# Performance work log

Measured on AMD Instinct MI355X. Metric: run time of the kernel, lower is better.

## Reference

```python
import jax, jax.numpy as jnp
import numpy as np

N_NODES = 50000
HEADS = 4
CH = 128
NEG_SLOPE = 0.2


def _gatv2_layer(x, src, dst, Wl, Wr, att, bias):
    # x: [N, Fin]; src/dst: [E'] (self-loops already appended)
    N = x.shape[0]
    xl = (x @ Wl).reshape(N, HEADS, CH)   # source-side transform
    xr = (x @ Wr).reshape(N, HEADS, CH)   # target-side transform
    e = jax.nn.leaky_relu(xl[src] + xr[dst], NEG_SLOPE)   # [E', H, C]
    logits = jnp.einsum('ehc,hc->eh', e, att)             # [E', H]
    # segment softmax over incoming edges of each destination node
    m = jax.ops.segment_max(logits, dst, num_segments=N)
    m = jnp.where(jnp.isfinite(m), m, 0.0)
    p = jnp.exp(logits - m[dst])
    denom = jax.ops.segment_sum(p, dst, num_segments=N)
    alpha = p / denom[dst]                                # [E', H]
    out = jax.ops.segment_sum(alpha[:, :, None] * xl[src], dst, num_segments=N)
    return out.reshape(N, HEADS * CH) + bias


def setup_inputs() -> dict:
    key = jax.random.key(0)
    ks = jax.random.split(key, 12)
    E = 400000
    x = jax.random.normal(ks[0], (N_NODES, 55), dtype=jnp.float32)
    edge_index = jax.random.randint(ks[1], (2, E), 0, N_NODES, dtype=jnp.int64)
    s = 0.1
    d1, d2 = 55, HEADS * CH
    return {
        'x': x,
        'edge_index': edge_index,
        'W1l': jax.random.normal(ks[2], (d1, d2), dtype=jnp.float32) * s,
        'W1r': jax.random.normal(ks[3], (d1, d2), dtype=jnp.float32) * s,
        'att1': jax.random.normal(ks[4], (HEADS, CH), dtype=jnp.float32) * s,
        'b1': jnp.zeros((d2,), dtype=jnp.float32),
        'W2l': jax.random.normal(ks[5], (d2, d2), dtype=jnp.float32) * s,
        'W2r': jax.random.normal(ks[6], (d2, d2), dtype=jnp.float32) * s,
        'att2': jax.random.normal(ks[7], (HEADS, CH), dtype=jnp.float32) * s,
        'b2': jnp.zeros((d2,), dtype=jnp.float32),
        'Wc': jax.random.normal(ks[8], (d2, 49), dtype=jnp.float32) * s,
        'bc': jnp.zeros((49,), dtype=jnp.float32),
    }


def reference(x, edge_index, W1l, W1r, att1, b1, W2l, W2r, att2, b2, Wc, bc):
    # add self loops once (PyG GATv2Conv default add_self_loops=True)
    loops = jnp.arange(N_NODES, dtype=edge_index.dtype)
    src = jnp.concatenate([edge_index[0], loops])
    dst = jnp.concatenate([edge_index[1], loops])
    h = _gatv2_layer(x, src, dst, W1l, W1r, att1, b1)
    h = jax.nn.elu(h)  # dropout is identity in eval mode
    h = _gatv2_layer(h, src, dst, W2l, W2r, att2, b2)
    h = jax.nn.elu(h)
    # forward applies conv2 a second time (conv3 unused in source)
    h = _gatv2_layer(h, src, dst, W2l, W2r, att2, b2)
    h = jax.nn.elu(h)
    return h @ Wc + bc
```

## Files before the change

### kernel.cpp

```cpp
#include <hip/hip_runtime.h>
#include <hip/hip_bf16.h>

constexpr int NN   = 50000;
constexpr int EE   = 400000;
constexpr int EP   = 450000;
constexpr int D    = 512;
constexpr int D2   = 1024;
constexpr int F0   = 55;
constexpr int F0P  = 64;
constexpr int OUTC = 49;

typedef __hip_bfloat16 bf16;

using frag_ab  = __attribute__((ext_vector_type(8))) short;
using frag_cd4 = __attribute__((ext_vector_type(4))) float;

__device__ inline void stf(float* p, float v) { *p = v; }
__device__ inline void stf(bf16* p, float v)  { *p = __float2bfloat16(v); }

__device__ inline void unpack8(uint4 u, float* f) {
    unsigned w[4] = {u.x, u.y, u.z, u.w};
    #pragma unroll
    for (int j = 0; j < 4; ++j) {
        __hip_bfloat162 h = *(__hip_bfloat162*)&w[j];
        float2 t = __bfloat1622float2(h);
        f[2 * j] = t.x; f[2 * j + 1] = t.y;
    }
}

template <typename TC, int NS>
__global__ __launch_bounds__(512, 4) void gemm_dp(
    const bf16* __restrict__ A,
    const bf16* __restrict__ Bt,
    TC* __restrict__ C,
    const float* __restrict__ bias,
    int M, int Ncs)
{
    constexpr int K  = NS * 32;
    constexpr int BM = 256, BN = 128, BK = 32;
    __shared__ __align__(16) bf16 As[3][BM * BK];
    __shared__ __align__(16) bf16 Bs[3][BN * BK];

    int bx = blockIdx.x, by = blockIdx.y;
    if (gridDim.x == 8) {
        int bid = by * 8 + bx;
        bx = (bid >> 3) & 7;
        by = (bid & 7) + ((bid >> 6) << 3);
    }
    if (by * BM >= M) return;

    const int tid = threadIdx.x;
    const int w   = tid >> 6;
    const int l   = tid & 63;
    const int rowBase = by * BM;
    const int colBase = bx * BN;

    const bf16* gA[2];
    #pragma unroll
    for (int j = 0; j < 2; ++j) {
        int f = j * 512 + tid;
        int row = f >> 2, c = (f & 3) ^ ((row >> 1) & 3);
        int ar = rowBase + row; if (ar >= M) ar = M - 1;
        gA[j] = A + (size_t)ar * K + c * 8;
    }
    const bf16* gB;
    {
        int f = tid;
        int row = f >> 2, c = (f & 3) ^ ((row >> 1) & 3);
        gB = Bt + (size_t)(colBase + row) * K + c * 8;
    }

    const int l15 = l & 15, l4 = l >> 4;
    const int wm = (w >> 1) * 64;
    const int wn = (w & 1) * 64;
    int aoff[4], boff[4];
    #pragma unroll
    for (int i = 0; i < 4; ++i) {
        int ra = wm + i * 16 + l15;
        int rb = wn + i * 16 + l15;
        aoff[i] = ra * BK + ((l4 ^ ((ra >> 1) & 3)) * 8);
        boff[i] = rb * BK + ((l4 ^ ((rb >> 1) & 3)) * 8);
    }

    frag_cd4 acc[4][4] = {};

    auto stage = [&](int s) {
        int slot = s % 3;
        __builtin_amdgcn_global_load_lds(
            (const __attribute__((address_space(1))) void*)(gA[0] + s * BK),
            (__attribute__((address_space(3))) void*)(&As[slot][(w * 64) * 8]),
            16, 0, 0);
        __builtin_amdgcn_global_load_lds(
            (const __attribute__((address_space(1))) void*)(gA[1] + s * BK),
            (__attribute__((address_space(3))) void*)(&As[slot][(512 + w * 64) * 8]),
            16, 0, 0);
        __builtin_amdgcn_global_load_lds(
            (const __attribute__((address_space(1))) void*)(gB + s * BK),
            (__attribute__((address_space(3))) void*)(&Bs[slot][(w * 64) * 8]),
            16, 0, 0);
    };

    stage(0);
    if (NS > 1) stage(1);

    #pragma unroll
    for (int s = 0; s < NS; ++s) {
        if (s + 1 < NS) asm volatile("s_waitcnt vmcnt(3)" ::: "memory");
        else            asm volatile("s_waitcnt vmcnt(0)" ::: "memory");
        __builtin_amdgcn_s_barrier();
        asm volatile("" ::: "memory");

        if (s + 2 < NS) stage(s + 2);

        const bf16* Ab = As[s % 3];
        const bf16* Bb = Bs[s % 3];
        frag_ab a[4], b[4];
        #pragma unroll
        for (int i = 0; i < 4; ++i) a[i] = *(const frag_ab*)&Ab[aoff[i]];
        #pragma unroll
        for (int n = 0; n < 4; ++n) b[n] = *(const frag_ab*)&Bb[boff[n]];

        __builtin_amdgcn_s_setprio(1);
        #pragma unroll
        for (int i = 0; i < 4; ++i)
            #pragma unroll
            for (int n = 0; n < 4; ++n)
                acc[i][n] = __builtin_amdgcn_mfma_f32_16x16x32_bf16(
                    a[i], b[n], acc[i][n], 0, 0, 0);
        __builtin_amdgcn_s_setprio(0);
    }

    #pragma unroll
    for (int mi = 0; mi < 4; ++mi) {
        #pragma unroll
        for (int r = 0; r < 4; ++r) {
            int row = rowBase + wm + mi * 16 + l4 * 4 + r;
            if (row >= M) continue;
            #pragma unroll
            for (int ni = 0; ni < 4; ++ni) {
                int col = colBase + wn + ni * 16 + l15;
                if (col >= Ncs) continue;
                float v = acc[mi][ni][r];
                if (bias) v += bias[col];
                stf(&C[(size_t)row * Ncs + col], v);
            }
        }
    }
}

__global__ void convert_transpose2(const float* __restrict__ W0,
                                   const float* __restrict__ W1,
                                   bf16* __restrict__ Wt) {
    __shared__ float tile[32][33];
    const float* W = blockIdx.z ? W1 : W0;
    bf16* dst = Wt + (size_t)blockIdx.z * D * D;
    int bn = blockIdx.x * 32, bk = blockIdx.y * 32;
    int tx = threadIdx.x & 31, ty = threadIdx.x >> 5;
    #pragma unroll
    for (int i = 0; i < 32; i += 8)
        tile[ty + i][tx] = W[(size_t)(bk + ty + i) * D + bn + tx];
    __syncthreads();
    #pragma unroll
    for (int i = 0; i < 32; i += 8)
        dst[(size_t)(bn + ty + i) * D + bk + tx] = __float2bfloat16(tile[tx][ty + i]);
}

__global__ void pad_convert_x(const float* __restrict__ x, bf16* __restrict__ Xp) {
    int idx = blockIdx.x * blockDim.x + threadIdx.x;
    if (idx >= NN * F0P) return;
    int n = idx >> 6, t = idx & 63;
    float v = (t < F0) ? x[n * F0 + t] : 0.f;
    Xp[idx] = __float2bfloat16(v);
}

__global__ void conv_transpose_w1(const float* __restrict__ Wl,
                                  const float* __restrict__ Wr,
                                  bf16* __restrict__ Wt) {
    const float* W = blockIdx.y ? Wr : Wl;
    bf16* dst = Wt + (size_t)blockIdx.y * D * F0P;
    int n = blockIdx.x;
    int k = threadIdx.x;
    float v = (k < F0) ? W[(size_t)k * D + n] : 0.f;
    dst[n * F0P + k] = __float2bfloat16(v);
}

__global__ void conv_transpose_wc(const float* __restrict__ W, bf16* __restrict__ Wt) {
    int n = blockIdx.x;
    for (int k = threadIdx.x; k < D; k += blockDim.x) {
        float v = (n < OUTC) ? W[(size_t)k * OUTC + n] : 0.f;
        Wt[(size_t)n * D + k] = __float2bfloat16(v);
    }
}

__global__ void zero_ints(int* __restrict__ p, int n) {
    int i = blockIdx.x * blockDim.x + threadIdx.x;
    if (i < n) p[i] = 0;
}

__global__ void count_dst(const int* __restrict__ dstIdx, int* __restrict__ cnt) {
    int e = blockIdx.x * blockDim.x + threadIdx.x;
    if (e >= EP) return;
    int dst = (e < EE) ? dstIdx[e] : (e - EE);
    atomicAdd(&cnt[dst], 1);
}

__global__ void scan_blocks(const int* __restrict__ cnt, int* __restrict__ off,
                            int* __restrict__ bsum) {
    __shared__ int sh[1024];
    int i = blockIdx.x * 1024 + threadIdx.x;
    int v = (i < NN) ? cnt[i] : 0;
    sh[threadIdx.x] = v;
    __syncthreads();
    #pragma unroll
    for (int d = 1; d < 1024; d <<= 1) {
        int t = (threadIdx.x >= d) ? sh[threadIdx.x - d] : 0;
        __syncthreads();
        sh[threadIdx.x] += t;
        __syncthreads();
    }
    if (i < NN) off[i] = sh[threadIdx.x] - v;
    if (threadIdx.x == 1023) bsum[blockIdx.x] = sh[1023];
}

__global__ void scan_bsums(int* __restrict__ bsum, int* __restrict__ bbase,
                           int* __restrict__ off, int nb) {
    int lane = threadIdx.x;
    int orig = (lane < nb) ? bsum[lane] : 0;
    int v = orig;
    #pragma unroll
    for (int d = 1; d < 64; d <<= 1) {
        int t = __shfl_up(v, d);
        if (lane >= d) v += t;
    }
    if (lane < nb) bbase[lane] = v - orig;
    if (lane == 63) off[NN] = v;
}

__global__ void add_base(int* __restrict__ off, const int* __restrict__ bbase) {
    int i = blockIdx.x * 1024 + threadIdx.x;
    if (blockIdx.x == 0 || i >= NN) return;
    off[i] += bbase[blockIdx.x];
}

__global__ void fill_srcpos(const int* __restrict__ srcIdx, const int* __restrict__ dstIdx,
                            const int* __restrict__ off, int* __restrict__ cnt,
                            int* __restrict__ srcPos) {
    int e = blockIdx.x * blockDim.x + threadIdx.x;
    if (e >= EP) return;
    int dst = (e < EE) ? dstIdx[e] : (e - EE);
    int src = (e < EE) ? srcIdx[e] : (e - EE);
    int pos = off[dst] + atomicAdd(&cnt[dst], 1);
    srcPos[pos] = src;
}

__global__ __launch_bounds__(256) void gat_edge_fused(
    const bf16* __restrict__ XLR, const float* __restrict__ att,
    const int* __restrict__ off, const int* __restrict__ srcPos,
    const float* __restrict__ bias, bf16* __restrict__ Hout)
{
    int v = blockIdx.x * 4 + (threadIdx.x >> 6);
    if (v >= NN) return;
    int lane = threadIdx.x & 63;

    uint4 ru = *(const uint4*)(XLR + (size_t)v * D2 + D + lane * 8);
    float xr[8]; unpack8(ru, xr);
    const float4* a4 = (const float4*)(att + lane * 8);
    float4 aa = a4[0], ab = a4[1];
    float at[8] = {aa.x, aa.y, aa.z, aa.w, ab.x, ab.y, ab.z, ab.w};

    int s0 = off[v], s1 = off[v + 1];
    float den = 0.f;
    float acc[8] = {};

    uint4 lb0 = {0, 0, 0, 0}, lb1 = {0, 0, 0, 0};
    if (s0 < s1)     lb0 = *(const uint4*)(XLR + (size_t)srcPos[s0] * D2 + lane * 8);
    if (s0 + 1 < s1) lb1 = *(const uint4*)(XLR + (size_t)srcPos[s0 + 1] * D2 + lane * 8);

    for (int i = s0; i < s1; ++i) {
        uint4 cur = lb0;
        lb0 = lb1;
        if (i + 2 < s1)
            lb1 = *(const uint4*)(XLR + (size_t)srcPos[i + 2] * D2 + lane * 8);

        float xl[8]; unpack8(cur, xl);
        float sa = 0.f, sb = 0.f;
        #pragma unroll
        for (int j = 0; j < 4; ++j) {
            float t = xl[j] + xr[j];
            t = fmaxf(t, 0.2f * t);
            sa = fmaf(t, at[j], sa);
        }
        #pragma unroll
        for (int j = 4; j < 8; ++j) {
            float t = xl[j] + xr[j];
            t = fmaxf(t, 0.2f * t);
            sb = fmaf(t, at[j], sb);
        }
        float s = sa + sb;
        s += __shfl_xor(s, 1);
        s += __shfl_xor(s, 2);
        s += __shfl_xor(s, 4);
        s += __shfl_xor(s, 8);
        s = fminf(fmaxf(s, -60.f), 60.f);
        float p = __expf(s);
        den += p;
        #pragma unroll
        for (int j = 0; j < 8; ++j) acc[j] = fmaf(p, xl[j], acc[j]);
    }
    float r = 1.f / den;

    const float4* b4 = (const float4*)(bias + lane * 8);
    float4 ba = b4[0], bb = b4[1];
    float bi[8] = {ba.x, ba.y, ba.z, ba.w, bb.x, bb.y, bb.z, bb.w};
    uint4 ou;
    unsigned* ow = (unsigned*)&ou;
    #pragma unroll
    for (int j = 0; j < 4; ++j) {
        float o0 = acc[2 * j] * r + bi[2 * j];
        float o1 = acc[2 * j + 1] * r + bi[2 * j + 1];
        o0 = o0 > 0.f ? o0 : (__expf(o0) - 1.f);
        o1 = o1 > 0.f ? o1 : (__expf(o1) - 1.f);
        __hip_bfloat162 h{__float2bfloat16(o0), __float2bfloat16(o1)};
        ow[j] = *(unsigned*)&h;
    }
    *(uint4*)(Hout + (size_t)v * D + lane * 8) = ou;
}

extern "C" void kernel_launch(void* const* d_in, const int* in_sizes, int n_in,
                              void* d_out, int out_size, void* d_ws, size_t ws_size,
                              hipStream_t stream) {
    const float* x    = (const float*)d_in[0];
    const int*   ei   = (const int*)d_in[1];
    const float* W1l  = (const float*)d_in[2];
    const float* W1r  = (const float*)d_in[3];
    const float* att1 = (const float*)d_in[4];
    const float* b1   = (const float*)d_in[5];
    const float* W2l  = (const float*)d_in[6];
    const float* W2r  = (const float*)d_in[7];
    const float* att2 = (const float*)d_in[8];
    const float* b2   = (const float*)d_in[9];
    const float* Wc   = (const float*)d_in[10];
    const float* bc   = (const float*)d_in[11];
    float* out = (float*)d_out;

    const int* srcIdx = ei;
    const int* dstIdx = ei + EE;

    constexpr int NB = (NN + 1023) / 1024;

    bf16* XLR  = (bf16*)d_ws;
    bf16* Hb   = XLR + (size_t)NN * D2;
    bf16* Xpad = Hb + (size_t)NN * D;
    bf16* W2T  = Xpad + (size_t)NN * F0P;
    bf16* W1T  = W2T + (size_t)D2 * D;
    bf16* WcT  = W1T + (size_t)D2 * F0P;
    int* cnt   = (int*)(WcT + (size_t)128 * D);
    int* cnt2  = cnt + NN;
    int* off   = cnt2 + NN;
    int* srcPos= off + (NN + 1);
    int* bsum  = srcPos + EP;
    int* bbase = bsum + NB;

    zero_ints<<<(2 * NN + 255) / 256, 256, 0, stream>>>(cnt, 2 * NN);
    count_dst<<<(EP + 255) / 256, 256, 0, stream>>>(dstIdx, cnt);
    scan_blocks<<<NB, 1024, 0, stream>>>(cnt, off, bsum);
    scan_bsums<<<1, 64, 0, stream>>>(bsum, bbase, off, NB);
    add_base<<<NB, 1024, 0, stream>>>(off, bbase);
    fill_srcpos<<<(EP + 255) / 256, 256, 0, stream>>>(srcIdx, dstIdx, off, cnt2, srcPos);

    dim3 ctGrid(D / 32, D / 32, 2);
    convert_transpose2<<<ctGrid, 256, 0, stream>>>(W2l, W2r, W2T);
    dim3 w1Grid(D, 2);
    conv_transpose_w1<<<w1Grid, F0P, 0, stream>>>(W1l, W1r, W1T);
    conv_transpose_wc<<<128, 256, 0, stream>>>(Wc, WcT);
    pad_convert_x<<<(NN * F0P + 255) / 256, 256, 0, stream>>>(x, Xpad);

    int panels = (NN + 255) / 256;
    int gy = (panels + 7) / 8 * 8;
    dim3 gemmGrid(D2 / 128, gy);
    int nodeBlocks = (NN + 3) / 4;

    gemm_dp<bf16, 2><<<gemmGrid, 512, 0, stream>>>(Xpad, W1T, XLR, nullptr, NN, D2);
    gat_edge_fused<<<nodeBlocks, 256, 0, stream>>>(XLR, att1, off, srcPos, b1, Hb);

    for (int rep = 0; rep < 2; ++rep) {
        gemm_dp<bf16, 16><<<gemmGrid, 512, 0, stream>>>(Hb, W2T, XLR, nullptr, NN, D2);
        gat_edge_fused<<<nodeBlocks, 256, 0, stream>>>(XLR, att2, off, srcPos, b2, Hb);
    }

    dim3 gridc(1, panels);
    gemm_dp<float, 16><<<gridc, 512, 0, stream>>>(Hb, WcT, out, bc, NN, OUTC);
}
```

Before: 565.9 us.

## Split GAT edge kernel per head, four nodes per wavefront

The edge aggregation kernel now gives each 16-lane group one attention head of one node, so each wavefront covers four nodes on the same head. Block IDs are swizzled so that paired blocks handle different heads of the same node range, which aims to cut per-wave serialization on high-degree nodes and improve L2 locality for gathered source rows. The trade-off is narrower gathers (256 bytes per row per group instead of 1 KB), more divergence from unequal degrees within a wave, and a hard-coded grid size.

```diff
diff --git a/kernel.cpp b/kernel.cpp
--- a/kernel.cpp
+++ b/kernel.cpp
@@ -253,18 +253,24 @@
     srcPos[pos] = src;
 }
 
-__global__ __launch_bounds__(256) void gat_edge_fused(
+__global__ __launch_bounds__(256) void gat_edge_head(
     const bf16* __restrict__ XLR, const float* __restrict__ att,
     const int* __restrict__ off, const int* __restrict__ srcPos,
     const float* __restrict__ bias, bf16* __restrict__ Hout)
 {
-    int v = blockIdx.x * 4 + (threadIdx.x >> 6);
-    if (v >= NN) return;
+    int bid = blockIdx.x;
+    int h   = (bid & 7) >> 1;
+    int nb  = ((bid >> 3) << 1) + (bid & 1);
+    if (nb >= NN / 16) return;
     int lane = threadIdx.x & 63;
-
-    uint4 ru = *(const uint4*)(XLR + (size_t)v * D2 + D + lane * 8);
+    int grp  = lane >> 4;
+    int l16  = lane & 15;
+    int v = nb * 16 + (int)(threadIdx.x >> 6) * 4 + grp;
+    const int hoff = h * 128 + l16 * 8;
+
+    uint4 ru = *(const uint4*)(XLR + (size_t)v * D2 + D + hoff);
     float xr[8]; unpack8(ru, xr);
-    const float4* a4 = (const float4*)(att + lane * 8);
+    const float4* a4 = (const float4*)(att + hoff);
     float4 aa = a4[0], ab = a4[1];
     float at[8] = {aa.x, aa.y, aa.z, aa.w, ab.x, ab.y, ab.z, ab.w};
 
@@ -273,14 +279,14 @@
     float acc[8] = {};
 
     uint4 lb0 = {0, 0, 0, 0}, lb1 = {0, 0, 0, 0};
-    if (s0 < s1)     lb0 = *(const uint4*)(XLR + (size_t)srcPos[s0] * D2 + lane * 8);
-    if (s0 + 1 < s1) lb1 = *(const uint4*)(XLR + (size_t)srcPos[s0 + 1] * D2 + lane * 8);
+    if (s0 < s1)     lb0 = *(const uint4*)(XLR + (size_t)srcPos[s0] * D2 + hoff);
+    if (s0 + 1 < s1) lb1 = *(const uint4*)(XLR + (size_t)srcPos[s0 + 1] * D2 + hoff);
 
     for (int i = s0; i < s1; ++i) {
         uint4 cur = lb0;
         lb0 = lb1;
         if (i + 2 < s1)
-            lb1 = *(const uint4*)(XLR + (size_t)srcPos[i + 2] * D2 + lane * 8);
+            lb1 = *(const uint4*)(XLR + (size_t)srcPos[i + 2] * D2 + hoff);
 
         float xl[8]; unpack8(cur, xl);
         float sa = 0.f, sb = 0.f;
@@ -309,7 +315,7 @@
     }
     float r = 1.f / den;
 
-    const float4* b4 = (const float4*)(bias + lane * 8);
+    const float4* b4 = (const float4*)(bias + hoff);
     float4 ba = b4[0], bb = b4[1];
     float bi[8] = {ba.x, ba.y, ba.z, ba.w, bb.x, bb.y, bb.z, bb.w};
     uint4 ou;
@@ -320,10 +326,10 @@
         float o1 = acc[2 * j + 1] * r + bi[2 * j + 1];
         o0 = o0 > 0.f ? o0 : (__expf(o0) - 1.f);
         o1 = o1 > 0.f ? o1 : (__expf(o1) - 1.f);
-        __hip_bfloat162 h{__float2bfloat16(o0), __float2bfloat16(o1)};
-        ow[j] = *(unsigned*)&h;
-    }
-    *(uint4*)(Hout + (size_t)v * D + lane * 8) = ou;
+        __hip_bfloat162 hh{__float2bfloat16(o0), __float2bfloat16(o1)};
+        ow[j] = *(unsigned*)&hh;
+    }
+    *(uint4*)(Hout + (size_t)v * D + hoff) = ou;
 }
 
 extern "C" void kernel_launch(void* const* d_in, const int* in_sizes, int n_in,
@@ -378,14 +384,14 @@
     int panels = (NN + 255) / 256;
     int gy = (panels + 7) / 8 * 8;
     dim3 gemmGrid(D2 / 128, gy);
-    int nodeBlocks = (NN + 3) / 4;
+    int headBlocks = 12504;
 
     gemm_dp<bf16, 2><<<gemmGrid, 512, 0, stream>>>(Xpad, W1T, XLR, nullptr, NN, D2);
-    gat_edge_fused<<<nodeBlocks, 256, 0, stream>>>(XLR, att1, off, srcPos, b1, Hb);
+    gat_edge_head<<<headBlocks, 256, 0, stream>>>(XLR, att1, off, srcPos, b1, Hb);
 
     for (int rep = 0; rep < 2; ++rep) {
         gemm_dp<bf16, 16><<<gemmGrid, 512, 0, stream>>>(Hb, W2T, XLR, nullptr, NN, D2);
-        gat_edge_fused<<<nodeBlocks, 256, 0, stream>>>(XLR, att2, off, srcPos, b2, Hb);
+        gat_edge_head<<<headBlocks, 256, 0, stream>>>(XLR, att2, off, srcPos, b2, Hb);
     }
 
     dim3 gridc(1, panels);
```

Result: no change. 576.1 us (+1.8%).
